# Optimization experiments

Measured on AMD Instinct MI355X. Metric: run time of the kernel, lower is better.

Reference implementation:

```python
import jax, jax.numpy as jnp
import numpy as np

B = 16        # decode batch (one query token per sequence)
H = 32        # query heads
HKV = 8       # kv heads (GQA)
D = 128       # head dim
BLOCK = 256   # kv-cache block size (from module: self.block_size = 256)
MAXBLK = 16   # blocks per sequence
MAXCTX = MAXBLK * BLOCK   # 4096
NBLK = 256    # total physical blocks
NSLOTS = NBLK * BLOCK     # 65536 slots
SCALE = 1.0 / float(np.sqrt(D))
EPS = 1e-8


def setup_inputs() -> dict:
    key = jax.random.key(0)
    ks = jax.random.split(key, 10)
    q = jax.random.normal(ks[0], (B, H, D), jnp.float32)
    k = jax.random.normal(ks[1], (B, HKV, D), jnp.float32)
    v = jax.random.normal(ks[2], (B, HKV, D), jnp.float32)
    # int8 quantized KV caches, layout [HKV, NSLOTS, D] per triton kernel strides
    k_cache = jax.random.randint(ks[3], (HKV, NSLOTS, D), -127, 128).astype(jnp.int8)
    v_cache = jax.random.randint(ks[4], (HKV, NSLOTS, D), -127, 128).astype(jnp.int8)
    # per-(head, slot) dequant scales, positive
    k_scale_cache = jax.random.uniform(ks[5], (HKV, NSLOTS), jnp.float32, 1e-4, 0.03)
    v_scale_cache = jax.random.uniform(ks[6], (HKV, NSLOTS), jnp.float32, 1e-4, 0.03)
    slot_mapping = jax.random.randint(ks[7], (B,), 0, NSLOTS)
    block_table = jax.random.randint(ks[8], (B, MAXBLK), 0, NBLK)
    context_lens = jax.random.randint(ks[9], (B,), 1, MAXCTX + 1)
    return dict(q=q, k=k, v=v, k_cache=k_cache, v_cache=v_cache,
                k_scale_cache=k_scale_cache, v_scale_cache=v_scale_cache,
                slot_mapping=slot_mapping, block_table=block_table,
                context_lens=context_lens)


def _quantize(x):
    # per-(token, head) abs-max int8 quantization, matching _store_quantkv_kernel
    s = jnp.maximum(jnp.max(jnp.abs(x), axis=-1) / 127.0, EPS)
    xi = jnp.clip(jnp.round(x / s[..., None]), -127.0, 127.0).astype(jnp.int8)
    return xi, s


def reference(q, k, v, k_cache, v_cache, k_scale_cache, v_scale_cache,
              slot_mapping, block_table, context_lens):
    G = H // HKV
    # --- gather + dequantize paged KV cache (decode_attn_quantkv_direct) ---
    pos = jnp.arange(MAXCTX)                               # [S]
    slots = block_table[:, pos // BLOCK] * BLOCK + (pos % BLOCK)  # [B, S]
    K = jnp.take(k_cache, slots, axis=1).astype(jnp.float32) \
        * jnp.take(k_scale_cache, slots, axis=1)[..., None]       # [HKV, B, S, D]
    V = jnp.take(v_cache, slots, axis=1).astype(jnp.float32) \
        * jnp.take(v_scale_cache, slots, axis=1)[..., None]       # [HKV, B, S, D]
    # --- attention: cached context tokens + current (unquantized) token ---
    qr = q.reshape(B, HKV, G, D)
    lc = jnp.einsum('bhgd,hbsd->bhgs', qr, K) * SCALE             # [B, HKV, G, S]
    valid = pos[None, :] < context_lens[:, None]                  # [B, S]
    lc = jnp.where(valid[:, None, None, :], lc, -jnp.inf)
    lcur = jnp.einsum('bhgd,bhd->bhg', qr, k) * SCALE             # current token
    logits = jnp.concatenate([lc, lcur[..., None]], axis=-1)      # [B, HKV, G, S+1]
    p = jax.nn.softmax(logits, axis=-1)
    o = jnp.einsum('bhgs,hbsd->bhgd', p[..., :MAXCTX], V) \
        + p[..., MAXCTX, None] * v[:, :, None, :]
    o = o.reshape(B, H, D)
    # --- fused quantized KV-cache store (store_quantkv) ---
    kq8, ks = _quantize(k)   # [B, HKV, D], [B, HKV]
    vq8, vs = _quantize(v)
    kc = k_cache.at[:, slot_mapping, :].set(jnp.transpose(kq8, (1, 0, 2)))
    vc = v_cache.at[:, slot_mapping, :].set(jnp.transpose(vq8, (1, 0, 2)))
    ksc = k_scale_cache.at[:, slot_mapping].set(ks.T)
    vsc = v_scale_cache.at[:, slot_mapping].set(vs.T)
    return (o, kc, vc, ksc, vsc)
```

## Files before the change

### kernel.cpp

```cpp
#include <hip/hip_runtime.h>
#include <hip/hip_fp16.h>
#include <stdint.h>

#define BB      16
#define HH      32
#define HKVN    8
#define GG      4
#define DD      128
#define BLK     256
#define MAXBLKN 16
#define MAXCTXN 4096
#define NSLOTSN 65536
#define ATT_SCALE 0.08838834764831845f
#define QEPS    1e-8f

#define NSPLIT  16
#define CHUNK   256

#define O_OFF   0
#define KC_OFF  65536
#define VC_OFF  (65536 + 67108864)
#define KSC_OFF (65536 + 2*67108864)
#define VSC_OFF (65536 + 2*67108864 + 524288)

#define WS_M    0
#define WS_L    8192
#define WS_O    16384

#define NREG    (HKVN * 256)
#define NOVF    (256 * HKVN)

typedef float f32x4 __attribute__((ext_vector_type(4)));

__global__ __launch_bounds__(256) void fused_kernel(
    const float* __restrict__ q,
    const int* __restrict__ k_cache, const int* __restrict__ v_cache,
    const float* __restrict__ k_scale, const float* __restrict__ v_scale,
    const int* __restrict__ block_table, const int* __restrict__ context_lens,
    float* __restrict__ ws, float* __restrict__ out) {
  const int bid = blockIdx.x;
  const int tid = threadIdx.x;

  __shared__ __align__(16) float q_s[GG][DD];
  __shared__ __half p_s[GG][CHUNK];
  __shared__ float racc[8][32][17];
  __shared__ float red[GG][4];
  __shared__ __align__(16) float ks_s[CHUNK];
  __shared__ __align__(16) float vs_s[CHUNK];
  __shared__ int minpair;
  __shared__ int ovf_p;

  const int lane = tid & 63;
  const int wid = tid >> 6;

  if (bid < NREG) {
    const int h = bid >> 8;
    const int p = bid & 255;
    if (tid == 0) minpair = 0x7fffffff;
    __syncthreads();
    if (block_table[tid] == p && (tid & 15) * CHUNK < context_lens[tid >> 4])
      atomicMin(&minpair, tid);
    __syncthreads();
    const int mp = minpair;
    const bool hp = (mp != 0x7fffffff);
    const int reg = h * NSLOTSN + p * BLK;

    if (tid < 64) {
      float4 w0 = ((const float4*)k_scale)[reg / 4 + tid];
      ((float4*)ks_s)[tid] = w0;
      f32x4 w; w.x = w0.x; w.y = w0.y; w.z = w0.z; w.w = w0.w;
      __builtin_nontemporal_store(w, (f32x4*)(out + KSC_OFF) + reg / 4 + tid);
    } else if (tid < 128) {
      float4 w0 = ((const float4*)v_scale)[reg / 4 + (tid - 64)];
      ((float4*)vs_s)[tid - 64] = w0;
      f32x4 w; w.x = w0.x; w.y = w0.y; w.z = w0.z; w.w = w0.w;
      __builtin_nontemporal_store(w, (f32x4*)(out + VSC_OFF) + reg / 4 + (tid - 64));
    }

    int b = 0, s = 0, n = 0;
    if (hp) {
      b = mp >> 4;
      s = mp & 15;
      n = min(CHUNK, context_lens[b] - s * CHUNK);
      for (int i = tid; i < GG * DD; i += 256)
        q_s[i >> 7][i & 127] = q[(b * HH + h * GG + (i >> 7)) * DD + (i & 127)];
    }
    __syncthreads();

    const int g5 = tid >> 5;
    const int j5 = tid & 31;
    const int d0 = 4 * j5;

    const int4* srcK = (const int4*)k_cache + (size_t)reg * 32;
    const int4* srcV = (const int4*)v_cache + (size_t)reg * 32;
    f32x4* dstK = (f32x4*)(out + KC_OFF) + (size_t)reg * 32;
    f32x4* dstV = (f32x4*)(out + VC_OFF) + (size_t)reg * 32;

    if (!hp) {
#pragma unroll 4
      for (int i = 0; i < 32; ++i) {
        const int u = i * 256 + tid;
        int4 w = srcK[u];
        f32x4 f;
        f.x = (float)w.x; f.y = (float)w.y; f.z = (float)w.z; f.w = (float)w.w;
        __builtin_nontemporal_store(f, dstK + u);
      }
#pragma unroll 4
      for (int i = 0; i < 32; ++i) {
        const int u = i * 256 + tid;
        int4 w = srcV[u];
        f32x4 f;
        f.x = (float)w.x; f.y = (float)w.y; f.z = (float)w.z; f.w = (float)w.w;
        __builtin_nontemporal_store(f, dstV + u);
      }
      return;
    }

    float qv[GG][4];
#pragma unroll
    for (int g = 0; g < GG; ++g)
#pragma unroll
      for (int j = 0; j < 4; ++j) qv[g][j] = q_s[g][d0 + j];
    float lmax[GG] = {-1e30f, -1e30f, -1e30f, -1e30f};
#pragma unroll 4
    for (int i = 0; i < 32; ++i) {
      const int u = i * 256 + tid;
      int4 w = srcK[u];
      f32x4 f;
      f.x = (float)w.x; f.y = (float)w.y; f.z = (float)w.z; f.w = (float)w.w;
      __builtin_nontemporal_store(f, dstK + u);
      const int tok = i * 8 + g5;
      float dot[GG];
#pragma unroll
      for (int g = 0; g < GG; ++g)
        dot[g] = qv[g][0] * f.x + qv[g][1] * f.y + qv[g][2] * f.z + qv[g][3] * f.w;
#pragma unroll
      for (int off = 1; off <= 16; off <<= 1)
#pragma unroll
        for (int g = 0; g < GG; ++g) dot[g] += __shfl_xor(dot[g], off);
      if (tok < n) {
        const float mult = ks_s[tok] * ATT_SCALE;
#pragma unroll
        for (int g = 0; g < GG; ++g) {
          float lg = dot[g] * mult;
          lmax[g] = fmaxf(lmax[g], lg);
          if (j5 == 0) p_s[g][tok] = __float2half(lg);
        }
      }
    }
#pragma unroll
    for (int g = 0; g < GG; ++g)
      for (int off = 32; off; off >>= 1)
        lmax[g] = fmaxf(lmax[g], __shfl_xor(lmax[g], off));
    if (lane == 0)
#pragma unroll
      for (int g = 0; g < GG; ++g) red[g][wid] = lmax[g];
    __syncthreads();
    float m[GG];
#pragma unroll
    for (int g = 0; g < GG; ++g)
      m[g] = fmaxf(fmaxf(red[g][0], red[g][1]), fmaxf(red[g][2], red[g][3]));

    float lsum[GG] = {0.f, 0.f, 0.f, 0.f};
    if (tid < n) {
#pragma unroll
      for (int g = 0; g < GG; ++g) {
        float e = __expf(__half2float(p_s[g][tid]) - m[g]);
        p_s[g][tid] = __float2half(e);
        lsum[g] += e;
      }
    }
#pragma unroll
    for (int g = 0; g < GG; ++g)
      for (int off = 32; off; off >>= 1) lsum[g] += __shfl_xor(lsum[g], off);
    __syncthreads();
    if (lane == 0)
#pragma unroll
      for (int g = 0; g < GG; ++g) red[g][wid] = lsum[g];
    __syncthreads();
    float l[GG];
#pragma unroll
    for (int g = 0; g < GG; ++g)
      l[g] = red[g][0] + red[g][1] + red[g][2] + red[g][3];

    float acc[GG][4] = {};
#pragma unroll 4
    for (int i = 0; i < 32; ++i) {
      const int u = i * 256 + tid;
      int4 w = srcV[u];
      f32x4 f;
      f.x = (float)w.x; f.y = (float)w.y; f.z = (float)w.z; f.w = (float)w.w;
      __builtin_nontemporal_store(f, dstV + u);
      const int tok = i * 8 + g5;
      if (tok < n) {
        const float vs = vs_s[tok];
        const float f0 = f.x * vs, f1 = f.y * vs, f2 = f.z * vs, f3 = f.w * vs;
#pragma unroll
        for (int g = 0; g < GG; ++g) {
          const float pw = __half2float(p_s[g][tok]);
          acc[g][0] += pw * f0; acc[g][1] += pw * f1;
          acc[g][2] += pw * f2; acc[g][3] += pw * f3;
        }
      }
    }
#pragma unroll
    for (int g = 0; g < GG; ++g)
#pragma unroll
      for (int j = 0; j < 4; ++j)
        racc[g5][j5][g * 4 + j] = acc[g][j];
    __syncthreads();
    const int bh = b * HKVN + h;
    for (int oidx = tid; oidx < 512; oidx += 256) {
      int gj = oidx & 15;
      int vl = oidx >> 4;
      float sacc = 0.f;
#pragma unroll
      for (int rr = 0; rr < 8; ++rr) sacc += racc[rr][vl][gj];
      int g = gj >> 2, j = gj & 3;
      ws[WS_O + (((bh * GG + g) * NSPLIT + s) * DD) + (vl * 4 + j)] = sacc;
    }
    if (tid == 0) {
#pragma unroll
      for (int g = 0; g < GG; ++g) {
        ws[WS_M + (bh * GG + g) * NSPLIT + s] = m[g];
        ws[WS_L + (bh * GG + g) * NSPLIT + s] = l[g];
      }
    }
    return;
  }

  {
    const int idx = bid - NREG;
    const int pi = idx >> 3;
    const int h = idx & 7;
    const int b = pi >> 4;
    const int s = pi & 15;
    if (s * CHUNK >= context_lens[b]) return;
    if (tid == 0) {
      minpair = 0x7fffffff;
      ovf_p = block_table[pi];
    }
    __syncthreads();
    const int p = ovf_p;
    if (block_table[tid] == p && (tid & 15) * CHUNK < context_lens[tid >> 4])
      atomicMin(&minpair, tid);
    __syncthreads();
    if (minpair == pi) return;

    const int bh = b * HKVN + h;
    const int ctx = context_lens[b];
    const int n = min(CHUNK, ctx - s * CHUNK);
    const int base = p * BLK;
    const int qlane = lane & 3;
    const int quad = lane >> 2;

    for (int i = tid; i < GG * DD; i += 256)
      q_s[i >> 7][i & 127] = q[(b * HH + h * GG + (i >> 7)) * DD + (i & 127)];
    __syncthreads();

    float lmax[GG] = {-1e30f, -1e30f, -1e30f, -1e30f};
#pragma unroll
    for (int it = 0; it < 4; ++it) {
      const int tok = it * 64 + wid * 16 + quad;
      const bool active = tok < n;
      const int slot = base + tok;
      float dot[GG] = {0.f, 0.f, 0.f, 0.f};
      if (active) {
        const int4* kr = (const int4*)(k_cache + (size_t)(h * NSLOTSN + slot) * DD);
#pragma unroll
        for (int kk = 0; kk < 8; ++kk) {
          int4 w = kr[qlane + 4 * kk];
          float k0 = (float)w.x, k1 = (float)w.y, k2 = (float)w.z, k3 = (float)w.w;
          const int c = (qlane + 4 * kk) * 4;
#pragma unroll
          for (int g = 0; g < GG; ++g) {
            float4 qv = *(const float4*)&q_s[g][c];
            dot[g] += qv.x * k0 + qv.y * k1 + qv.z * k2 + qv.w * k3;
          }
        }
      }
#pragma unroll
      for (int g = 0; g < GG; ++g) {
        dot[g] += __shfl_xor(dot[g], 1);
        dot[g] += __shfl_xor(dot[g], 2);
      }
      if (active && qlane == 0) {
        float mult = k_scale[h * NSLOTSN + slot] * ATT_SCALE;
#pragma unroll
        for (int g = 0; g < GG; ++g) {
          float lg = dot[g] * mult;
          p_s[g][tok] = __float2half(lg);
          lmax[g] = fmaxf(lmax[g], lg);
        }
      }
    }
#pragma unroll
    for (int g = 0; g < GG; ++g)
      for (int off = 32; off; off >>= 1)
        lmax[g] = fmaxf(lmax[g], __shfl_xor(lmax[g], off));
    if (lane == 0)
#pragma unroll
      for (int g = 0; g < GG; ++g) red[g][wid] = lmax[g];
    __syncthreads();
    float m[GG];
#pragma unroll
    for (int g = 0; g < GG; ++g)
      m[g] = fmaxf(fmaxf(red[g][0], red[g][1]), fmaxf(red[g][2], red[g][3]));

    float lsum[GG] = {0.f, 0.f, 0.f, 0.f};
    if (tid < n) {
#pragma unroll
      for (int g = 0; g < GG; ++g) {
        float e = __expf(__half2float(p_s[g][tid]) - m[g]);
        p_s[g][tid] = __float2half(e);
        lsum[g] += e;
      }
    }
#pragma unroll
    for (int g = 0; g < GG; ++g)
      for (int off = 32; off; off >>= 1) lsum[g] += __shfl_xor(lsum[g], off);
    __syncthreads();
    if (lane == 0)
#pragma unroll
      for (int g = 0; g < GG; ++g) red[g][wid] = lsum[g];
    __syncthreads();
    float l[GG];
#pragma unroll
    for (int g = 0; g < GG; ++g)
      l[g] = red[g][0] + red[g][1] + red[g][2] + red[g][3];

    const int vlane = tid & 31;
    const int grp = tid >> 5;
    float acc[GG][4] = {};
    const int vhb = h * NSLOTSN;
#pragma unroll 4
    for (int i = grp; i < n; i += 8) {
      int slot = base + i;
      float vs = v_scale[vhb + slot];
      int4 w = *(const int4*)(v_cache + (size_t)(vhb + slot) * DD + 4 * vlane);
      float v0 = (float)w.x * vs, v1 = (float)w.y * vs,
            v2 = (float)w.z * vs, v3 = (float)w.w * vs;
#pragma unroll
      for (int g = 0; g < GG; ++g) {
        float pw = __half2float(p_s[g][i]);
        acc[g][0] += pw * v0; acc[g][1] += pw * v1;
        acc[g][2] += pw * v2; acc[g][3] += pw * v3;
      }
    }
#pragma unroll
    for (int g = 0; g < GG; ++g)
#pragma unroll
      for (int j = 0; j < 4; ++j)
        racc[grp][vlane][g * 4 + j] = acc[g][j];
    __syncthreads();
    for (int oidx = tid; oidx < 512; oidx += 256) {
      int gj = oidx & 15;
      int vl = oidx >> 4;
      float sacc = 0.f;
#pragma unroll
      for (int rr = 0; rr < 8; ++rr) sacc += racc[rr][vl][gj];
      int g = gj >> 2, j = gj & 3;
      ws[WS_O + (((bh * GG + g) * NSPLIT + s) * DD) + (vl * 4 + j)] = sacc;
    }
    if (tid == 0) {
#pragma unroll
      for (int g = 0; g < GG; ++g) {
        ws[WS_M + (bh * GG + g) * NSPLIT + s] = m[g];
        ws[WS_L + (bh * GG + g) * NSPLIT + s] = l[g];
      }
    }
  }
}

__global__ __launch_bounds__(128) void finish_kernel(
    const float* __restrict__ q, const float* __restrict__ kin,
    const float* __restrict__ vin, const int* __restrict__ slot_mapping,
    const int* __restrict__ context_lens, float* __restrict__ out,
    const float* __restrict__ ws) {
  const int d = threadIdx.x;
  __shared__ float red[DD];
  __shared__ float lcur_s[GG];

  if (blockIdx.x < 128) {
    const int bh = blockIdx.x;
    const int h = bh & 7;
    const int b = bh >> 3;
    const int ctx = context_lens[b];
    const int nsp = (ctx + CHUNK - 1) / CHUNK;
    if (d < GG) {
      float dc = 0.f;
      const float* qp = q + (b * HH + h * GG + d) * DD;
      const float* kp = kin + (b * HKVN + h) * DD;
      for (int j = 0; j < DD; ++j) dc += qp[j] * kp[j];
      lcur_s[d] = dc * ATT_SCALE;
    }
    __syncthreads();
    float vcur = vin[(b * HKVN + h) * DD + d];
#pragma unroll
    for (int g = 0; g < GG; ++g) {
      float lc = lcur_s[g];
      float M = lc;
      for (int s = 0; s < nsp; ++s)
        M = fmaxf(M, ws[WS_M + (bh * GG + g) * NSPLIT + s]);
      float denom = __expf(lc - M);
      float o = denom * vcur;
      for (int s = 0; s < nsp; ++s) {
        float w = __expf(ws[WS_M + (bh * GG + g) * NSPLIT + s] - M);
        denom += ws[WS_L + (bh * GG + g) * NSPLIT + s] * w;
        o += ws[WS_O + ((bh * GG + g) * NSPLIT + s) * DD + d] * w;
      }
      out[O_OFF + (b * HH + h * GG + g) * DD + d] = o / denom;
    }
  } else {
    const int sid = blockIdx.x - 128;
    const int b = sid >> 3;
    const int h = sid & 7;
    const int slot = slot_mapping[b];
    for (int b2 = b + 1; b2 < BB; ++b2)
      if (slot_mapping[b2] == slot) return;

    float xk = kin[(b * HKVN + h) * DD + d];
    red[d] = fabsf(xk);
    __syncthreads();
    for (int off = 64; off; off >>= 1) {
      if (d < off) red[d] = fmaxf(red[d], red[d + off]);
      __syncthreads();
    }
    float sk = fmaxf(red[0] / 127.0f, QEPS);
    __syncthreads();
    float qk = fminf(fmaxf(rintf(xk / sk), -127.0f), 127.0f);
    out[KC_OFF + (h * NSLOTSN + slot) * DD + d] = qk;
    if (d == 0) out[KSC_OFF + h * NSLOTSN + slot] = sk;

    float xv = vin[(b * HKVN + h) * DD + d];
    red[d] = fabsf(xv);
    __syncthreads();
    for (int off = 64; off; off >>= 1) {
      if (d < off) red[d] = fmaxf(red[d], red[d + off]);
      __syncthreads();
    }
    float sv = fmaxf(red[0] / 127.0f, QEPS);
    float qv = fminf(fmaxf(rintf(xv / sv), -127.0f), 127.0f);
    out[VC_OFF + (h * NSLOTSN + slot) * DD + d] = qv;
    if (d == 0) out[VSC_OFF + h * NSLOTSN + slot] = sv;
  }
}

extern "C" void kernel_launch(void* const* d_in, const int* in_sizes, int n_in,
                              void* d_out, int out_size, void* d_ws, size_t ws_size,
                              hipStream_t stream) {
  const float* q = (const float*)d_in[0];
  const float* k = (const float*)d_in[1];
  const float* v = (const float*)d_in[2];
  const int* k_cache = (const int*)d_in[3];
  const int* v_cache = (const int*)d_in[4];
  const float* k_scale = (const float*)d_in[5];
  const float* v_scale = (const float*)d_in[6];
  const int* slot_mapping = (const int*)d_in[7];
  const int* block_table = (const int*)d_in[8];
  const int* context_lens = (const int*)d_in[9];
  float* out = (float*)d_out;
  float* ws = (float*)d_ws;

  hipLaunchKernelGGL(fused_kernel, dim3(NREG + NOVF), dim3(256), 0, stream,
                     q, k_cache, v_cache, k_scale, v_scale,
                     block_table, context_lens, ws, out);
  hipLaunchKernelGGL(finish_kernel, dim3(256), dim3(128), 0, stream,
                     q, k, v, slot_mapping, context_lens, out, ws);
}
```

Baseline: 260.9 us.

## Fuse K and V passes into single online-softmax loop per chunk

Replaces the three-phase chunk attention (logits pass over K, block softmax with barriers, separate pass over V) with one loop that reads K and V together and keeps a per-row online softmax state (running max, sum, accumulator). The eight row-group partial states are then merged in shared memory with exp-weighted rescaling. Non-attention copy blocks also switch to nontemporal loads. This removes two block barriers and the fp16 probability scratch, and overlaps K and V loads. In exchange it adds per-token exp and rescale work and branch divergence, and register pressure goes up.

```diff
diff --git a/kernel.cpp b/kernel.cpp
--- a/kernel.cpp
+++ b/kernel.cpp
@@ -31,6 +31,7 @@
 #define NOVF    (256 * HKVN)
 
 typedef float f32x4 __attribute__((ext_vector_type(4)));
+typedef int   i32x4 __attribute__((ext_vector_type(4)));
 
 __global__ __launch_bounds__(256) void fused_kernel(
     const float* __restrict__ q,
@@ -44,7 +45,10 @@
   __shared__ __align__(16) float q_s[GG][DD];
   __shared__ __half p_s[GG][CHUNK];
   __shared__ float racc[8][32][17];
-  __shared__ float red[GG][4];
+  __shared__ float red[GG][8];
+  __shared__ float red_l[GG][8];
+  __shared__ float wgt[GG][8];
+  __shared__ float Mv[GG], Lv[GG];
   __shared__ __align__(16) float ks_s[CHUNK];
   __shared__ __align__(16) float vs_s[CHUNK];
   __shared__ int minpair;
@@ -91,8 +95,8 @@
     const int j5 = tid & 31;
     const int d0 = 4 * j5;
 
-    const int4* srcK = (const int4*)k_cache + (size_t)reg * 32;
-    const int4* srcV = (const int4*)v_cache + (size_t)reg * 32;
+    const i32x4* srcK = (const i32x4*)k_cache + (size_t)reg * 32;
+    const i32x4* srcV = (const i32x4*)v_cache + (size_t)reg * 32;
     f32x4* dstK = (f32x4*)(out + KC_OFF) + (size_t)reg * 32;
     f32x4* dstV = (f32x4*)(out + VC_OFF) + (size_t)reg * 32;
 
@@ -100,7 +104,7 @@
 #pragma unroll 4
       for (int i = 0; i < 32; ++i) {
         const int u = i * 256 + tid;
-        int4 w = srcK[u];
+        i32x4 w = __builtin_nontemporal_load(srcK + u);
         f32x4 f;
         f.x = (float)w.x; f.y = (float)w.y; f.z = (float)w.z; f.w = (float)w.w;
         __builtin_nontemporal_store(f, dstK + u);
@@ -108,7 +112,7 @@
 #pragma unroll 4
       for (int i = 0; i < 32; ++i) {
         const int u = i * 256 + tid;
-        int4 w = srcV[u];
+        i32x4 w = __builtin_nontemporal_load(srcV + u);
         f32x4 f;
         f.x = (float)w.x; f.y = (float)w.y; f.z = (float)w.z; f.w = (float)w.w;
         __builtin_nontemporal_store(f, dstV + u);
@@ -121,109 +125,93 @@
     for (int g = 0; g < GG; ++g)
 #pragma unroll
       for (int j = 0; j < 4; ++j) qv[g][j] = q_s[g][d0 + j];
-    float lmax[GG] = {-1e30f, -1e30f, -1e30f, -1e30f};
-#pragma unroll 4
+    float m[GG], l[GG] = {0.f, 0.f, 0.f, 0.f};
+    float acc[GG][4] = {};
+#pragma unroll
+    for (int g = 0; g < GG; ++g) m[g] = -1e30f;
+
+#pragma unroll 2
     for (int i = 0; i < 32; ++i) {
       const int u = i * 256 + tid;
-      int4 w = srcK[u];
-      f32x4 f;
-      f.x = (float)w.x; f.y = (float)w.y; f.z = (float)w.z; f.w = (float)w.w;
-      __builtin_nontemporal_store(f, dstK + u);
+      i32x4 wk = srcK[u];
+      i32x4 wv = srcV[u];
+      f32x4 fk;
+      fk.x = (float)wk.x; fk.y = (float)wk.y; fk.z = (float)wk.z; fk.w = (float)wk.w;
+      __builtin_nontemporal_store(fk, dstK + u);
+      f32x4 fv;
+      fv.x = (float)wv.x; fv.y = (float)wv.y; fv.z = (float)wv.z; fv.w = (float)wv.w;
+      __builtin_nontemporal_store(fv, dstV + u);
+      float dot[GG];
+#pragma unroll
+      for (int g = 0; g < GG; ++g)
+        dot[g] = qv[g][0] * fk.x + qv[g][1] * fk.y + qv[g][2] * fk.z + qv[g][3] * fk.w;
+#pragma unroll
+      for (int off = 1; off <= 16; off <<= 1)
+#pragma unroll
+        for (int g = 0; g < GG; ++g) dot[g] += __shfl_xor(dot[g], off);
       const int tok = i * 8 + g5;
-      float dot[GG];
-#pragma unroll
-      for (int g = 0; g < GG; ++g)
-        dot[g] = qv[g][0] * f.x + qv[g][1] * f.y + qv[g][2] * f.z + qv[g][3] * f.w;
-#pragma unroll
-      for (int off = 1; off <= 16; off <<= 1)
-#pragma unroll
-        for (int g = 0; g < GG; ++g) dot[g] += __shfl_xor(dot[g], off);
       if (tok < n) {
         const float mult = ks_s[tok] * ATT_SCALE;
+        const float vsc = vs_s[tok];
+        const float v0 = fv.x * vsc, v1 = fv.y * vsc,
+                    v2 = fv.z * vsc, v3 = fv.w * vsc;
 #pragma unroll
         for (int g = 0; g < GG; ++g) {
-          float lg = dot[g] * mult;
-          lmax[g] = fmaxf(lmax[g], lg);
-          if (j5 == 0) p_s[g][tok] = __float2half(lg);
+          const float lg = dot[g] * mult;
+          if (lg > m[g]) {
+            const float sc = __expf(m[g] - lg);
+            l[g] *= sc;
+            acc[g][0] *= sc; acc[g][1] *= sc;
+            acc[g][2] *= sc; acc[g][3] *= sc;
+            m[g] = lg;
+          }
+          const float e = __expf(lg - m[g]);
+          l[g] += e;
+          acc[g][0] += e * v0; acc[g][1] += e * v1;
+          acc[g][2] += e * v2; acc[g][3] += e * v3;
         }
       }
     }
-#pragma unroll
-    for (int g = 0; g < GG; ++g)
-      for (int off = 32; off; off >>= 1)
-        lmax[g] = fmaxf(lmax[g], __shfl_xor(lmax[g], off));
-    if (lane == 0)
-#pragma unroll
-      for (int g = 0; g < GG; ++g) red[g][wid] = lmax[g];
-    __syncthreads();
-    float m[GG];
-#pragma unroll
-    for (int g = 0; g < GG; ++g)
-      m[g] = fmaxf(fmaxf(red[g][0], red[g][1]), fmaxf(red[g][2], red[g][3]));
-
-    float lsum[GG] = {0.f, 0.f, 0.f, 0.f};
-    if (tid < n) {
-#pragma unroll
-      for (int g = 0; g < GG; ++g) {
-        float e = __expf(__half2float(p_s[g][tid]) - m[g]);
-        p_s[g][tid] = __float2half(e);
-        lsum[g] += e;
-      }
-    }
-#pragma unroll
-    for (int g = 0; g < GG; ++g)
-      for (int off = 32; off; off >>= 1) lsum[g] += __shfl_xor(lsum[g], off);
-    __syncthreads();
-    if (lane == 0)
-#pragma unroll
-      for (int g = 0; g < GG; ++g) red[g][wid] = lsum[g];
-    __syncthreads();
-    float l[GG];
-#pragma unroll
-    for (int g = 0; g < GG; ++g)
-      l[g] = red[g][0] + red[g][1] + red[g][2] + red[g][3];
-
-    float acc[GG][4] = {};
-#pragma unroll 4
-    for (int i = 0; i < 32; ++i) {
-      const int u = i * 256 + tid;
-      int4 w = srcV[u];
-      f32x4 f;
-      f.x = (float)w.x; f.y = (float)w.y; f.z = (float)w.z; f.w = (float)w.w;
-      __builtin_nontemporal_store(f, dstV + u);
-      const int tok = i * 8 + g5;
-      if (tok < n) {
-        const float vs = vs_s[tok];
-        const float f0 = f.x * vs, f1 = f.y * vs, f2 = f.z * vs, f3 = f.w * vs;
-#pragma unroll
-        for (int g = 0; g < GG; ++g) {
-          const float pw = __half2float(p_s[g][tok]);
-          acc[g][0] += pw * f0; acc[g][1] += pw * f1;
-          acc[g][2] += pw * f2; acc[g][3] += pw * f3;
-        }
-      }
-    }
-#pragma unroll
-    for (int g = 0; g < GG; ++g)
-#pragma unroll
-      for (int j = 0; j < 4; ++j)
-        racc[g5][j5][g * 4 + j] = acc[g][j];
+
+    if (j5 == 0) {
+#pragma unroll
+      for (int g = 0; g < GG; ++g) { red[g][g5] = m[g]; red_l[g][g5] = l[g]; }
+    }
+#pragma unroll
+    for (int g = 0; g < GG; ++g)
+#pragma unroll
+      for (int j = 0; j < 4; ++j) racc[g5][j5][g * 4 + j] = acc[g][j];
+    __syncthreads();
+    if (tid < GG) {
+      const int g = tid;
+      float M = red[g][0];
+#pragma unroll
+      for (int r = 1; r < 8; ++r) M = fmaxf(M, red[g][r]);
+      float L = 0.f;
+#pragma unroll
+      for (int r = 0; r < 8; ++r) {
+        const float w = __expf(red[g][r] - M);
+        wgt[g][r] = w;
+        L += w * red_l[g][r];
+      }
+      Mv[g] = M; Lv[g] = L;
+    }
     __syncthreads();
     const int bh = b * HKVN + h;
     for (int oidx = tid; oidx < 512; oidx += 256) {
-      int gj = oidx & 15;
-      int vl = oidx >> 4;
+      const int gj = oidx & 15;
+      const int vl = oidx >> 4;
+      const int g = gj >> 2;
       float sacc = 0.f;
 #pragma unroll
-      for (int rr = 0; rr < 8; ++rr) sacc += racc[rr][vl][gj];
-      int g = gj >> 2, j = gj & 3;
-      ws[WS_O + (((bh * GG + g) * NSPLIT + s) * DD) + (vl * 4 + j)] = sacc;
+      for (int r = 0; r < 8; ++r) sacc += wgt[g][r] * racc[r][vl][gj];
+      ws[WS_O + (((bh * GG + g) * NSPLIT + s) * DD) + (vl * 4 + (gj & 3))] = sacc;
     }
     if (tid == 0) {
 #pragma unroll
       for (int g = 0; g < GG; ++g) {
-        ws[WS_M + (bh * GG + g) * NSPLIT + s] = m[g];
-        ws[WS_L + (bh * GG + g) * NSPLIT + s] = l[g];
+        ws[WS_M + (bh * GG + g) * NSPLIT + s] = Mv[g];
+        ws[WS_L + (bh * GG + g) * NSPLIT + s] = Lv[g];
       }
     }
     return;
```

Result: faster. 227.7 us (-12.7%).
